# Performance work log

Measured on AMD Instinct MI355X. Metric: run time of the kernel, lower is better.

The kernel has to match this reference:

```python
import jax, jax.numpy as jnp
import numpy as np

N_NODES = 100000
N_GRAPHS = 256
N_EDGES = 800000


def gcn_conv(x, W, b, src, dst):
    """PyG GCNConv: self-loops + symmetric deg^-1/2 normalization + scatter-add."""
    h = x @ W  # [N, F_out]
    # degree on graph with self-loops (edge weight 1)
    deg = jax.ops.segment_sum(jnp.ones((src.shape[0],), h.dtype), dst,
                              num_segments=N_NODES) + 1.0
    dinv = jax.lax.rsqrt(deg)  # deg^-1/2, deg >= 1 so finite
    norm = dinv[src] * dinv[dst]  # [E]
    msg = h[src] * norm[:, None]  # gather + scale, [E, F_out]
    agg = jax.ops.segment_sum(msg, dst, num_segments=N_NODES)
    # self-loop contribution: dinv[i]^2 * h[i]
    agg = agg + h * (dinv * dinv)[:, None]
    return agg + b


def setup_inputs() -> dict:
    key = jax.random.key(0)
    ks = jax.random.split(key, 16)
    inp = {
        "x": jax.random.normal(ks[0], (N_NODES, 114), jnp.float32),
        "edge_index": jax.random.randint(ks[1], (2, N_EDGES), 0, N_NODES, jnp.int64)
        if jax.config.jax_enable_x64 else jax.random.randint(ks[1], (2, N_EDGES), 0, N_NODES, jnp.int32),
        "batch": jnp.sort(jax.random.randint(ks[2], (N_NODES,), 0, N_GRAPHS,
                                             jnp.int32)),
        "W1": jax.random.normal(ks[3], (114, 230), jnp.float32) * 0.09,
        "b1": jax.random.normal(ks[4], (230,), jnp.float32) * 0.01,
        "W2": jax.random.normal(ks[5], (230, 115), jnp.float32) * 0.07,
        "b2": jax.random.normal(ks[6], (115,), jnp.float32) * 0.01,
        "Wg": jax.random.normal(ks[7], (115, 64), jnp.float32) * 0.09,
        "bg": jax.random.normal(ks[8], (64,), jnp.float32) * 0.01,
        "Wf": jax.random.normal(ks[9], (64, 32), jnp.float32) * 0.12,
        "bf": jax.random.normal(ks[10], (32,), jnp.float32) * 0.01,
        "Wo": jax.random.normal(ks[11], (32, 1), jnp.float32) * 0.17,
        "bo": jax.random.normal(ks[12], (1,), jnp.float32) * 0.01,
    }
    return inp


def reference(x, edge_index, batch, W1, b1, W2, b2, Wg, bg, Wf, bf, Wo, bo):
    src, dst = edge_index[0], edge_index[1]
    h = jax.nn.relu(gcn_conv(x, W1, b1, src, dst))
    # dropout p=0.2 is identity at inference (training=False)
    h = jax.nn.relu(gcn_conv(h, W2, b2, src, dst))
    # global max pool over graphs; h >= 0 after relu so clamp empty segments to 0
    pooled = jax.ops.segment_max(h, batch, num_segments=N_GRAPHS)
    pooled = jnp.maximum(pooled, 0.0)  # [G, 115]
    g = jax.nn.relu(pooled @ Wg + bg)
    g = jax.nn.relu(g @ Wf + bf)
    return g @ Wo + bo  # [G, 1]
```

## Files before the change

kernel.cpp:

```cpp
#include <hip/hip_runtime.h>
#include <hip/hip_bf16.h>
#include <hip/hip_fp16.h>

#define NN 100000
#define NG 256
#define NE 800000

constexpr int F0 = 114;
constexpr int F1 = 230;
constexpr int F2 = 115;
constexpr int MPAD = 100096;

typedef _Float16 __attribute__((ext_vector_type(8))) f16x8;
typedef __attribute__((ext_vector_type(4))) float f32x4;
typedef __attribute__((ext_vector_type(8))) unsigned short u16x8;

__device__ __forceinline__ unsigned short f2h_bits(float x) {
  _Float16 h = (_Float16)x;
  return __builtin_bit_cast(unsigned short, h);
}
__device__ __forceinline__ float h_bits2f(unsigned short u) {
  return (float)__builtin_bit_cast(_Float16, u);
}


__global__ void k_count(const int* __restrict__ dst, int* __restrict__ cnt) {
  int e = blockIdx.x * blockDim.x + threadIdx.x;
  if (e < NE) atomicAdd(&cnt[dst[e]], 1);
}

__global__ void k_dinv(const int* __restrict__ cnt, float* __restrict__ dinv) {
  int i = blockIdx.x * blockDim.x + threadIdx.x;
  if (i < NN) dinv[i] = rsqrtf((float)cnt[i] + 1.0f);
}

constexpr int SCAN_T = 256;
constexpr int SCAN_E = 1024;
constexpr int NB = (NN + SCAN_E - 1) / SCAN_E;

__global__ void k_scan1(const int* __restrict__ cnt, int* __restrict__ off,
                        int* __restrict__ bsum) {
  __shared__ int s[SCAN_T];
  int b = blockIdx.x, t = threadIdx.x;
  int base = b * SCAN_E + t * 4;
  int v0 = 0, v1 = 0, v2 = 0, v3 = 0;
  if (base + 0 < NN) v0 = cnt[base + 0];
  if (base + 1 < NN) v1 = cnt[base + 1];
  if (base + 2 < NN) v2 = cnt[base + 2];
  if (base + 3 < NN) v3 = cnt[base + 3];
  int sum = v0 + v1 + v2 + v3;
  s[t] = sum;
  __syncthreads();
  for (int ofs = 1; ofs < SCAN_T; ofs <<= 1) {
    int x = (t >= ofs) ? s[t - ofs] : 0;
    __syncthreads();
    s[t] += x;
    __syncthreads();
  }
  int excl = s[t] - sum;
  if (base + 0 < NN) off[base + 0] = excl;
  if (base + 1 < NN) off[base + 1] = excl + v0;
  if (base + 2 < NN) off[base + 2] = excl + v0 + v1;
  if (base + 3 < NN) off[base + 3] = excl + v0 + v1 + v2;
  if (t == SCAN_T - 1) bsum[b] = s[t];
}

__global__ void k_scan2(int* bsum) {
  if (threadIdx.x == 0) {
    int run = 0;
    for (int i = 0; i < NB; ++i) { int v = bsum[i]; bsum[i] = run; run += v; }
  }
}

__global__ void k_scan3(int* __restrict__ off, const int* __restrict__ bsum,
                        int* __restrict__ cur) {
  int i = blockIdx.x * blockDim.x + threadIdx.x;
  if (i < NN) {
    int v = off[i] + bsum[i / SCAN_E];
    off[i] = v;
    cur[i] = v;
  }
  if (i == NN) off[NN] = NE;
}

__global__ void k_place(const int* __restrict__ src, const int* __restrict__ dst,
                        int* __restrict__ cur, int* __restrict__ srcs) {
  int e = blockIdx.x * blockDim.x + threadIdx.x;
  if (e >= NE) return;
  int p = atomicAdd(&cur[dst[e]], 1);
  srcs[p] = src[e];
}


__global__ void k_prepx(const float* __restrict__ x, const float* __restrict__ dinv,
                        unsigned short* __restrict__ xd) {
  int n = blockIdx.x, f = threadIdx.x;
  float v = (f < F0) ? x[(size_t)n * F0 + f] * dinv[n] : 0.0f;
  xd[(size_t)n * 128 + f] = f2h_bits(v);
}


template <bool POOL>
__global__ __launch_bounds__(256) void k_gatherw(
    const unsigned short* __restrict__ tab, const float* __restrict__ dinv,
    const int* __restrict__ off, const int* __restrict__ srcs,
    const float* __restrict__ b2, const int* __restrict__ batch,
    unsigned short* __restrict__ outh, float* __restrict__ pooled) {
  __shared__ float smax[4][128];
  __shared__ int sg[4];
  int w = threadIdx.x >> 6, lane = threadIdx.x & 63;
  int n = blockIdx.x * 4 + w;
  int grp = lane >> 4, sub = lane & 15;
  int fb = sub * 8;

  float acc[8] = {0.f, 0.f, 0.f, 0.f, 0.f, 0.f, 0.f, 0.f};
  int j0 = off[n], j1 = off[n + 1];
  for (int base = j0; base <= j1; base += 16) {
    int row[4];
    u16x8 v[4];
    bool has[4];
#pragma unroll
    for (int c = 0; c < 4; ++c) {
      int je = base + c * 4 + grp;
      row[c] = (je < j1) ? srcs[je] : ((je == j1) ? n : -1);
      has[c] = row[c] >= 0;
    }
#pragma unroll
    for (int c = 0; c < 4; ++c)
      if (has[c]) v[c] = *(const u16x8*)&tab[(size_t)row[c] * 128 + fb];
#pragma unroll
    for (int c = 0; c < 4; ++c)
      if (has[c]) {
#pragma unroll
        for (int u = 0; u < 8; ++u) acc[u] += h_bits2f(v[c][u]);
      }
  }
#pragma unroll
  for (int u = 0; u < 8; ++u) {
    acc[u] += __shfl_xor(acc[u], 16);
    acc[u] += __shfl_xor(acc[u], 32);
  }
  float dn = dinv[n];

  if constexpr (!POOL) {
    if (grp == 0) {
      u16x8 o;
#pragma unroll
      for (int u = 0; u < 8; ++u) o[u] = f2h_bits(acc[u] * dn);
      *(u16x8*)&outh[(size_t)n * 128 + fb] = o;
    }
  } else {
    if (grp == 0) {
#pragma unroll
      for (int u = 0; u < 8; ++u) {
        int f = fb + u;
        float bb = (f < F2) ? b2[f] : 0.0f;
        smax[w][f] = fmaxf(acc[u] * dn + bb, 0.0f);
      }
      if (sub == 0) sg[w] = batch[n];
    }
    __syncthreads();
    int t = threadIdx.x;
    if (t < 128) {
      int g0 = sg[0];
      bool same = (sg[1] == g0) & (sg[2] == g0) & (sg[3] == g0);
      if (same) {
        float m = fmaxf(fmaxf(smax[0][t], smax[1][t]),
                        fmaxf(smax[2][t], smax[3][t]));
        if (t < F2 && m > 0.0f)
          atomicMax((int*)&pooled[g0 * F2 + t], __float_as_int(m));
      } else {
        for (int ww = 0; ww < 4; ++ww) {
          float m = smax[ww][t];
          if (t < F2 && m > 0.0f)
            atomicMax((int*)&pooled[sg[ww] * F2 + t], __float_as_int(m));
        }
      }
    }
  }
}


__global__ void k_prepB(const float* __restrict__ W, unsigned short* __restrict__ Bh,
                        unsigned short* __restrict__ Bl, int K, int N, int KP) {
  int n = blockIdx.x, k = threadIdx.x;
  float v = (k < K && n < N) ? W[(size_t)k * N + n] : 0.0f;
  unsigned short h = f2h_bits(v);
  unsigned short l = f2h_bits(v - h_bits2f(h));
  Bh[(size_t)n * KP + k] = h;
  Bl[(size_t)n * KP + k] = l;
}


__global__ __launch_bounds__(256) void k_fused(
    const unsigned short* __restrict__ A,
    const unsigned short* __restrict__ B1h, const unsigned short* __restrict__ B1l,
    const unsigned short* __restrict__ B2h, const unsigned short* __restrict__ B2l,
    const float* __restrict__ b1, const float* __restrict__ dscale,
    unsigned short* __restrict__ td) {
  constexpr int LDH = 264;
  constexpr int LD = 72;
  __shared__ unsigned short h1s[64 * LDH];
  __shared__ unsigned short As[64 * LD];
  __shared__ unsigned short Bs[2][128 * LD];

  int t = threadIdx.x;
  int m0 = blockIdx.x * 64;
  int lane = t & 63, w = t >> 6;
  int r = lane & 15, kb = (lane >> 4) * 8;
  int rq = (lane >> 4) * 4;
  int wc = w * 32;

  int arow = t >> 2, aq = t & 3;
  int brow = t >> 1, bs = t & 1;

  for (int h = 0; h < 2; ++h) {
    f32x4 acc[4][2];
#pragma unroll
    for (int i = 0; i < 4; ++i)
#pragma unroll
      for (int j = 0; j < 2; ++j) acc[i][j] = (f32x4){0.f, 0.f, 0.f, 0.f};

    for (int kc = 0; kc < 2; ++kc) {
      __syncthreads();
      {
        size_t ga = (size_t)(m0 + arow) * 128 + kc * 64 + aq * 16;
        *(u16x8*)&As[arow * LD + aq * 16]     = *(const u16x8*)&A[ga];
        *(u16x8*)&As[arow * LD + aq * 16 + 8] = *(const u16x8*)&A[ga + 8];
        size_t gb = (size_t)(h * 128 + brow) * 128 + kc * 64 + bs * 32;
        int lo = brow * LD + bs * 32;
#pragma unroll
        for (int v = 0; v < 4; ++v) {
          *(u16x8*)&Bs[0][lo + v * 8] = *(const u16x8*)&B1h[gb + v * 8];
          *(u16x8*)&Bs[1][lo + v * 8] = *(const u16x8*)&B1l[gb + v * 8];
        }
      }
      __syncthreads();
#pragma unroll
      for (int ks = 0; ks < 2; ++ks) {
        int col = ks * 32 + kb;
        f16x8 a[4], bh[2], bl[2];
#pragma unroll
        for (int i = 0; i < 4; ++i) a[i] = *(const f16x8*)&As[(i * 16 + r) * LD + col];
#pragma unroll
        for (int j = 0; j < 2; ++j) {
          bh[j] = *(const f16x8*)&Bs[0][(wc + j * 16 + r) * LD + col];
          bl[j] = *(const f16x8*)&Bs[1][(wc + j * 16 + r) * LD + col];
        }
#pragma unroll
        for (int i = 0; i < 4; ++i)
#pragma unroll
          for (int j = 0; j < 2; ++j)
            acc[i][j] = __builtin_amdgcn_mfma_f32_16x16x32_f16(a[i], bl[j], acc[i][j], 0, 0, 0);
#pragma unroll
        for (int i = 0; i < 4; ++i)
#pragma unroll
          for (int j = 0; j < 2; ++j)
            acc[i][j] = __builtin_amdgcn_mfma_f32_16x16x32_f16(a[i], bh[j], acc[i][j], 0, 0, 0);
      }
    }
#pragma unroll
    for (int i = 0; i < 4; ++i)
#pragma unroll
      for (int j = 0; j < 2; ++j) {
        int nl = wc + j * 16 + r;
        int n = h * 128 + nl;
        float bb = (n < F1) ? b1[n] : 0.0f;
#pragma unroll
        for (int q = 0; q < 4; ++q) {
          int ml = i * 16 + rq + q;
          float v = (n < F1) ? fmaxf(acc[i][j][q] + bb, 0.0f) : 0.0f;
          h1s[ml * LDH + n] = f2h_bits(v);
        }
      }
  }

  f32x4 acc2[4][2];
#pragma unroll
  for (int i = 0; i < 4; ++i)
#pragma unroll
    for (int j = 0; j < 2; ++j) acc2[i][j] = (f32x4){0.f, 0.f, 0.f, 0.f};

  for (int kc = 0; kc < 4; ++kc) {
    __syncthreads();
    {
      size_t gb = (size_t)brow * 256 + kc * 64 + bs * 32;
      int lo = brow * LD + bs * 32;
#pragma unroll
      for (int v = 0; v < 4; ++v) {
        *(u16x8*)&Bs[0][lo + v * 8] = *(const u16x8*)&B2h[gb + v * 8];
        *(u16x8*)&Bs[1][lo + v * 8] = *(const u16x8*)&B2l[gb + v * 8];
      }
    }
    __syncthreads();
#pragma unroll
    for (int ks = 0; ks < 2; ++ks) {
      int colA = kc * 64 + ks * 32 + kb;
      int colB = ks * 32 + kb;
      f16x8 a[4], bh[2], bl[2];
#pragma unroll
      for (int i = 0; i < 4; ++i) a[i] = *(const f16x8*)&h1s[(i * 16 + r) * LDH + colA];
#pragma unroll
      for (int j = 0; j < 2; ++j) {
        bh[j] = *(const f16x8*)&Bs[0][(wc + j * 16 + r) * LD + colB];
        bl[j] = *(const f16x8*)&Bs[1][(wc + j * 16 + r) * LD + colB];
      }
#pragma unroll
      for (int i = 0; i < 4; ++i)
#pragma unroll
        for (int j = 0; j < 2; ++j)
          acc2[i][j] = __builtin_amdgcn_mfma_f32_16x16x32_f16(a[i], bl[j], acc2[i][j], 0, 0, 0);
#pragma unroll
      for (int i = 0; i < 4; ++i)
#pragma unroll
        for (int j = 0; j < 2; ++j)
          acc2[i][j] = __builtin_amdgcn_mfma_f32_16x16x32_f16(a[i], bh[j], acc2[i][j], 0, 0, 0);
    }
  }

  __syncthreads();
  constexpr int SW = 136;
  unsigned short* sw = h1s;
#pragma unroll
  for (int i = 0; i < 4; ++i)
#pragma unroll
    for (int j = 0; j < 2; ++j) {
      int nl = wc + j * 16 + r;
#pragma unroll
      for (int q = 0; q < 4; ++q) {
        int ml = i * 16 + rq + q;
        float v = acc2[i][j][q] * dscale[m0 + ml];
        sw[ml * SW + nl] = f2h_bits(v);
      }
    }
  __syncthreads();
  {
    int row = t >> 2, sgm = t & 3;
    const unsigned short* s = &sw[row * SW + sgm * 32];
    size_t dst = (size_t)(m0 + row) * 128 + sgm * 32;
#pragma unroll
    for (int v = 0; v < 4; ++v)
      *(u16x8*)&td[dst + v * 8] = *(const u16x8*)&s[v * 8];
  }
}


__global__ void k_mlp(const float* __restrict__ pooled,
                      const float* __restrict__ Wg, const float* __restrict__ bg,
                      const float* __restrict__ Wf, const float* __restrict__ bf,
                      const float* __restrict__ Wo, const float* __restrict__ bo,
                      float* __restrict__ out) {
  __shared__ float sp[F2];
  __shared__ float sg[64];
  __shared__ float sf[32];
  int g = blockIdx.x, t = threadIdx.x;
  for (int f = t; f < F2; f += 64) sp[f] = pooled[g * F2 + f];
  __syncthreads();
  float a = bg[t];
  for (int k = 0; k < F2; ++k) a += sp[k] * Wg[k * 64 + t];
  sg[t] = fmaxf(a, 0.0f);
  __syncthreads();
  if (t < 32) {
    float c = bf[t];
    for (int k = 0; k < 64; ++k) c += sg[k] * Wf[k * 32 + t];
    sf[t] = fmaxf(c, 0.0f);
  }
  __syncthreads();
  if (t == 0) {
    float c = bo[0];
    for (int k = 0; k < 32; ++k) c += sf[k] * Wo[k];
    out[g] = c;
  }
}


extern "C" void kernel_launch(void* const* d_in, const int* in_sizes, int n_in,
                              void* d_out, int out_size, void* d_ws, size_t ws_size,
                              hipStream_t stream) {
  const float* x  = (const float*)d_in[0];
  const int* ei   = (const int*)d_in[1];
  const int* batch = (const int*)d_in[2];
  const float* W1 = (const float*)d_in[3];
  const float* b1 = (const float*)d_in[4];
  const float* W2 = (const float*)d_in[5];
  const float* b2 = (const float*)d_in[6];
  const float* Wg = (const float*)d_in[7];
  const float* bg = (const float*)d_in[8];
  const float* Wf = (const float*)d_in[9];
  const float* bf = (const float*)d_in[10];
  const float* Wo = (const float*)d_in[11];
  const float* bo = (const float*)d_in[12];
  const int* src = ei;
  const int* dst = ei + NE;

  char* p = (char*)d_ws;
  auto alloc4 = [&](size_t units) { void* r = p; p += units * 4; return r; };
  float* dinv  = (float*)alloc4(100224);
  int* cnt     = (int*)alloc4(100224);
  int* off     = (int*)alloc4(100352);
  int* cur     = (int*)alloc4(100224);
  int* bsum    = (int*)alloc4(128);
  int* srcs    = (int*)alloc4(NE);
  unsigned short* xd   = (unsigned short*)alloc4((size_t)NN * 128 / 2);
  unsigned short* aggX = (unsigned short*)alloc4((size_t)MPAD * 128 / 2);
  unsigned short* td   = (unsigned short*)alloc4((size_t)MPAD * 128 / 2);
  unsigned short* Bt1h = (unsigned short*)alloc4(256 * 128 / 2);
  unsigned short* Bt1l = (unsigned short*)alloc4(256 * 128 / 2);
  unsigned short* Bt2h = (unsigned short*)alloc4(128 * 256 / 2);
  unsigned short* Bt2l = (unsigned short*)alloc4(128 * 256 / 2);
  float* pooled = (float*)alloc4((size_t)NG * F2);

  hipMemsetAsync(cnt, 0, 100224 * sizeof(int), stream);
  hipMemsetAsync(pooled, 0, (size_t)NG * F2 * sizeof(float), stream);

  k_count<<<(NE + 255) / 256, 256, 0, stream>>>(dst, cnt);
  k_dinv<<<(NN + 255) / 256, 256, 0, stream>>>(cnt, dinv);
  k_scan1<<<NB, SCAN_T, 0, stream>>>(cnt, off, bsum);
  k_scan2<<<1, 64, 0, stream>>>(bsum);
  k_scan3<<<(NN + 256) / 256, 256, 0, stream>>>(off, bsum, cur);
  k_place<<<(NE + 255) / 256, 256, 0, stream>>>(src, dst, cur, srcs);

  k_prepB<<<256, 128, 0, stream>>>(W1, Bt1h, Bt1l, F0, F1, 128);
  k_prepB<<<128, 256, 0, stream>>>(W2, Bt2h, Bt2l, F1, F2, 256);

  k_prepx<<<NN, 128, 0, stream>>>(x, dinv, xd);
  k_gatherw<false><<<NN / 4, 256, 0, stream>>>(xd, dinv, off, srcs,
                                               nullptr, nullptr, aggX, nullptr);

  k_fused<<<MPAD / 64, 256, 0, stream>>>(aggX, Bt1h, Bt1l, Bt2h, Bt2l,
                                         b1, dinv, td);

  k_gatherw<true><<<NN / 4, 256, 0, stream>>>(td, dinv, off, srcs,
                                              b2, batch, nullptr, pooled);

  k_mlp<<<NG, 64, 0, stream>>>(pooled, Wg, bg, Wf, bf, Wo, bo, (float*)d_out);
}
```

Measured before the change: 307.9 us.

## Restructure fused GEMM with register-prefetched B tiles, swizzled LDS, and interleaved layer-2 chunks

The fused two-layer GEMM kernel is rewritten. B tiles are prefetched into registers one stage ahead, and A fragments are loaded directly from global memory into registers instead of being staged through LDS. Each 128-column half of layer 1 now feeds straight into the matching slice of the layer-2 reduction, so the h1 buffer only holds 128 columns. LDS use drops to 48KB with an XOR swizzle replacing padding, and launch bounds now request 3 blocks per CU for occupancy; the serial single-thread block-sum scan also becomes a wave-shuffle scan. The risks are higher register pressure from the prefetch buffers and more barriers.

```diff
diff --git a/kernel.cpp b/kernel.cpp
--- a/kernel.cpp
+++ b/kernel.cpp
@@ -66,10 +66,18 @@
 }
 
 __global__ void k_scan2(int* bsum) {
-  if (threadIdx.x == 0) {
-    int run = 0;
-    for (int i = 0; i < NB; ++i) { int v = bsum[i]; bsum[i] = run; run += v; }
-  }
+  __shared__ int ws[2];
+  int t = threadIdx.x;
+  int v = (t < NB) ? bsum[t] : 0;
+  int orig = v;
+  for (int o = 1; o < 64; o <<= 1) {
+    int x = __shfl_up(v, o, 64);
+    if ((t & 63) >= o) v += x;
+  }
+  if ((t & 63) == 63) ws[t >> 6] = v;
+  __syncthreads();
+  if (t >= 64) v += ws[0];
+  if (t < NB) bsum[t] = v - orig;
 }
 
 __global__ void k_scan3(int* __restrict__ off, const int* __restrict__ bsum,
@@ -192,155 +200,189 @@
 }
 
 
-__global__ __launch_bounds__(256) void k_fused(
+__global__ __launch_bounds__(256, 3) void k_fused(
     const unsigned short* __restrict__ A,
     const unsigned short* __restrict__ B1h, const unsigned short* __restrict__ B1l,
     const unsigned short* __restrict__ B2h, const unsigned short* __restrict__ B2l,
     const float* __restrict__ b1, const float* __restrict__ dscale,
     unsigned short* __restrict__ td) {
-  constexpr int LDH = 264;
-  constexpr int LD = 72;
-  __shared__ unsigned short h1s[64 * LDH];
-  __shared__ unsigned short As[64 * LD];
-  __shared__ unsigned short Bs[2][128 * LD];
-
-  int t = threadIdx.x;
-  int m0 = blockIdx.x * 64;
-  int lane = t & 63, w = t >> 6;
-  int r = lane & 15, kb = (lane >> 4) * 8;
-  int rq = (lane >> 4) * 4;
-  int wc = w * 32;
-
-  int arow = t >> 2, aq = t & 3;
-  int brow = t >> 1, bs = t & 1;
-
-  for (int h = 0; h < 2; ++h) {
-    f32x4 acc[4][2];
+  __shared__ char lds[49152];
+  char* h1B = lds;
+  char* Bs0 = lds + 16384;
+  char* Bs1 = lds + 32768;
+
+  const int t = threadIdx.x;
+  const int m0 = blockIdx.x * 64;
+  const int lane = t & 63, w = t >> 6;
+  const int r = lane & 15;
+  const int kq = lane >> 4;
+  const int kb2 = kq * 16;
+  const int kbu = kq * 8;
+  const int rq = kq * 4;
+  const int wc = w * 32;
+  const int brow = t >> 1, bseg = t & 1;
+  const int rb = brow * 128, swb = (brow & 7) << 4;
+
+  const unsigned short* Ath = A + (size_t)(m0 + r) * 128 + kbu;
+
+  u16x8 Ph[4], Pl[4];
+  f16x8 a[4][2];
+  f32x4 acc[4][2], acc2[4][2];
+#pragma unroll
+  for (int i = 0; i < 4; ++i)
+#pragma unroll
+    for (int j = 0; j < 2; ++j) {
+      acc[i][j] = (f32x4){0.f, 0.f, 0.f, 0.f};
+      acc2[i][j] = (f32x4){0.f, 0.f, 0.f, 0.f};
+    }
+
+  auto issueB = [&](const unsigned short* Gh, const unsigned short* Gl, size_t base) {
+#pragma unroll
+    for (int v = 0; v < 4; ++v) {
+      Ph[v] = *(const u16x8*)&Gh[base + v * 8];
+      Pl[v] = *(const u16x8*)&Gl[base + v * 8];
+    }
+  };
+  auto commitB = [&]() {
+#pragma unroll
+    for (int v = 0; v < 4; ++v) {
+      const int bo = (bseg * 64 + v * 16) ^ swb;
+      *(u16x8*)(Bs0 + rb + bo) = Ph[v];
+      *(u16x8*)(Bs1 + rb + bo) = Pl[v];
+    }
+  };
+  auto loadA = [&](int kc) {
 #pragma unroll
     for (int i = 0; i < 4; ++i)
 #pragma unroll
+      for (int ks = 0; ks < 2; ++ks)
+        a[i][ks] = *(const f16x8*)&Ath[i * 2048 + kc * 64 + ks * 32];
+  };
+  auto mfma1 = [&]() {
+#pragma unroll
+    for (int ks = 0; ks < 2; ++ks) {
+      f16x8 bh[2], bl[2];
+#pragma unroll
+      for (int j = 0; j < 2; ++j) {
+        const int row = wc + j * 16 + r;
+        const int bo = (ks * 64 + kb2) ^ ((row & 7) << 4);
+        bh[j] = *(const f16x8*)(Bs0 + row * 128 + bo);
+        bl[j] = *(const f16x8*)(Bs1 + row * 128 + bo);
+      }
+#pragma unroll
+      for (int i = 0; i < 4; ++i)
+#pragma unroll
+        for (int j = 0; j < 2; ++j)
+          acc[i][j] = __builtin_amdgcn_mfma_f32_16x16x32_f16(a[i][ks], bl[j], acc[i][j], 0, 0, 0);
+#pragma unroll
+      for (int i = 0; i < 4; ++i)
+#pragma unroll
+        for (int j = 0; j < 2; ++j)
+          acc[i][j] = __builtin_amdgcn_mfma_f32_16x16x32_f16(a[i][ks], bh[j], acc[i][j], 0, 0, 0);
+    }
+  };
+  auto mfma2 = [&](int kc) {
+#pragma unroll
+    for (int ks = 0; ks < 2; ++ks) {
+      f16x8 ah[4], bh[2], bl[2];
+#pragma unroll
+      for (int i = 0; i < 4; ++i) {
+        const int row = i * 16 + r;
+        ah[i] = *(const f16x8*)(h1B + row * 256 +
+                                ((kc * 128 + ks * 64 + kb2) ^ ((row & 7) << 4)));
+      }
+#pragma unroll
+      for (int j = 0; j < 2; ++j) {
+        const int row = wc + j * 16 + r;
+        const int bo = (ks * 64 + kb2) ^ ((row & 7) << 4);
+        bh[j] = *(const f16x8*)(Bs0 + row * 128 + bo);
+        bl[j] = *(const f16x8*)(Bs1 + row * 128 + bo);
+      }
+#pragma unroll
+      for (int i = 0; i < 4; ++i)
+#pragma unroll
+        for (int j = 0; j < 2; ++j)
+          acc2[i][j] = __builtin_amdgcn_mfma_f32_16x16x32_f16(ah[i], bl[j], acc2[i][j], 0, 0, 0);
+#pragma unroll
+      for (int i = 0; i < 4; ++i)
+#pragma unroll
+        for (int j = 0; j < 2; ++j)
+          acc2[i][j] = __builtin_amdgcn_mfma_f32_16x16x32_f16(ah[i], bh[j], acc2[i][j], 0, 0, 0);
+    }
+  };
+  auto writeH1 = [&](int h) {
+#pragma unroll
+    for (int i = 0; i < 4; ++i)
+#pragma unroll
+      for (int j = 0; j < 2; ++j) {
+        const int nl = wc + j * 16 + r;
+        const int n = h * 128 + nl;
+        const bool val = n < F1;
+        const float bb = val ? b1[n] : 0.0f;
+#pragma unroll
+        for (int q = 0; q < 4; ++q) {
+          const int ml = i * 16 + rq + q;
+          const float v = val ? fmaxf(acc[i][j][q] + bb, 0.0f) : 0.0f;
+          *(unsigned short*)(h1B + ml * 256 + ((nl * 2) ^ ((ml & 7) << 4))) = f2h_bits(v);
+        }
+      }
+  };
+  auto zacc = [&]() {
+#pragma unroll
+    for (int i = 0; i < 4; ++i)
+#pragma unroll
       for (int j = 0; j < 2; ++j) acc[i][j] = (f32x4){0.f, 0.f, 0.f, 0.f};
-
-    for (int kc = 0; kc < 2; ++kc) {
-      __syncthreads();
-      {
-        size_t ga = (size_t)(m0 + arow) * 128 + kc * 64 + aq * 16;
-        *(u16x8*)&As[arow * LD + aq * 16]     = *(const u16x8*)&A[ga];
-        *(u16x8*)&As[arow * LD + aq * 16 + 8] = *(const u16x8*)&A[ga + 8];
-        size_t gb = (size_t)(h * 128 + brow) * 128 + kc * 64 + bs * 32;
-        int lo = brow * LD + bs * 32;
-#pragma unroll
-        for (int v = 0; v < 4; ++v) {
-          *(u16x8*)&Bs[0][lo + v * 8] = *(const u16x8*)&B1h[gb + v * 8];
-          *(u16x8*)&Bs[1][lo + v * 8] = *(const u16x8*)&B1l[gb + v * 8];
-        }
-      }
-      __syncthreads();
-#pragma unroll
-      for (int ks = 0; ks < 2; ++ks) {
-        int col = ks * 32 + kb;
-        f16x8 a[4], bh[2], bl[2];
-#pragma unroll
-        for (int i = 0; i < 4; ++i) a[i] = *(const f16x8*)&As[(i * 16 + r) * LD + col];
-#pragma unroll
-        for (int j = 0; j < 2; ++j) {
-          bh[j] = *(const f16x8*)&Bs[0][(wc + j * 16 + r) * LD + col];
-          bl[j] = *(const f16x8*)&Bs[1][(wc + j * 16 + r) * LD + col];
-        }
-#pragma unroll
-        for (int i = 0; i < 4; ++i)
-#pragma unroll
-          for (int j = 0; j < 2; ++j)
-            acc[i][j] = __builtin_amdgcn_mfma_f32_16x16x32_f16(a[i], bl[j], acc[i][j], 0, 0, 0);
-#pragma unroll
-        for (int i = 0; i < 4; ++i)
-#pragma unroll
-          for (int j = 0; j < 2; ++j)
-            acc[i][j] = __builtin_amdgcn_mfma_f32_16x16x32_f16(a[i], bh[j], acc[i][j], 0, 0, 0);
-      }
-    }
-#pragma unroll
-    for (int i = 0; i < 4; ++i)
-#pragma unroll
-      for (int j = 0; j < 2; ++j) {
-        int nl = wc + j * 16 + r;
-        int n = h * 128 + nl;
-        float bb = (n < F1) ? b1[n] : 0.0f;
-#pragma unroll
-        for (int q = 0; q < 4; ++q) {
-          int ml = i * 16 + rq + q;
-          float v = (n < F1) ? fmaxf(acc[i][j][q] + bb, 0.0f) : 0.0f;
-          h1s[ml * LDH + n] = f2h_bits(v);
-        }
-      }
-  }
-
-  f32x4 acc2[4][2];
+  };
+  auto B1BASE = [&](int h, int kc) {
+    return (size_t)(h * 128 + brow) * 128 + kc * 64 + bseg * 32;
+  };
+  auto B2BASE = [&](int h, int kc) {
+    return (size_t)brow * 256 + h * 128 + kc * 64 + bseg * 32;
+  };
+
+  issueB(B1h, B1l, B1BASE(0, 0));
+
+  commitB(); loadA(0); issueB(B1h, B1l, B1BASE(0, 1));
+  __syncthreads(); mfma1();
+  __syncthreads(); commitB(); loadA(1); issueB(B2h, B2l, B2BASE(0, 0));
+  __syncthreads(); mfma1(); writeH1(0);
+  __syncthreads(); commitB(); issueB(B2h, B2l, B2BASE(0, 1));
+  __syncthreads(); mfma2(0);
+  __syncthreads(); commitB(); issueB(B1h, B1l, B1BASE(1, 0));
+  __syncthreads(); mfma2(1);
+  zacc();
+  __syncthreads(); commitB(); loadA(0); issueB(B1h, B1l, B1BASE(1, 1));
+  __syncthreads(); mfma1();
+  __syncthreads(); commitB(); loadA(1); issueB(B2h, B2l, B2BASE(1, 0));
+  __syncthreads(); mfma1(); writeH1(1);
+  __syncthreads(); commitB(); issueB(B2h, B2l, B2BASE(1, 1));
+  __syncthreads(); mfma2(0);
+  __syncthreads(); commitB();
+  __syncthreads(); mfma2(1);
+
+  __syncthreads();
 #pragma unroll
   for (int i = 0; i < 4; ++i)
 #pragma unroll
-    for (int j = 0; j < 2; ++j) acc2[i][j] = (f32x4){0.f, 0.f, 0.f, 0.f};
-
-  for (int kc = 0; kc < 4; ++kc) {
-    __syncthreads();
-    {
-      size_t gb = (size_t)brow * 256 + kc * 64 + bs * 32;
-      int lo = brow * LD + bs * 32;
-#pragma unroll
-      for (int v = 0; v < 4; ++v) {
-        *(u16x8*)&Bs[0][lo + v * 8] = *(const u16x8*)&B2h[gb + v * 8];
-        *(u16x8*)&Bs[1][lo + v * 8] = *(const u16x8*)&B2l[gb + v * 8];
-      }
-    }
-    __syncthreads();
-#pragma unroll
-    for (int ks = 0; ks < 2; ++ks) {
-      int colA = kc * 64 + ks * 32 + kb;
-      int colB = ks * 32 + kb;
-      f16x8 a[4], bh[2], bl[2];
-#pragma unroll
-      for (int i = 0; i < 4; ++i) a[i] = *(const f16x8*)&h1s[(i * 16 + r) * LDH + colA];
-#pragma unroll
-      for (int j = 0; j < 2; ++j) {
-        bh[j] = *(const f16x8*)&Bs[0][(wc + j * 16 + r) * LD + colB];
-        bl[j] = *(const f16x8*)&Bs[1][(wc + j * 16 + r) * LD + colB];
-      }
-#pragma unroll
-      for (int i = 0; i < 4; ++i)
-#pragma unroll
-        for (int j = 0; j < 2; ++j)
-          acc2[i][j] = __builtin_amdgcn_mfma_f32_16x16x32_f16(a[i], bl[j], acc2[i][j], 0, 0, 0);
-#pragma unroll
-      for (int i = 0; i < 4; ++i)
-#pragma unroll
-        for (int j = 0; j < 2; ++j)
-          acc2[i][j] = __builtin_amdgcn_mfma_f32_16x16x32_f16(a[i], bh[j], acc2[i][j], 0, 0, 0);
-    }
-  }
-
-  __syncthreads();
-  constexpr int SW = 136;
-  unsigned short* sw = h1s;
-#pragma unroll
-  for (int i = 0; i < 4; ++i)
-#pragma unroll
     for (int j = 0; j < 2; ++j) {
-      int nl = wc + j * 16 + r;
+      const int nl = wc + j * 16 + r;
 #pragma unroll
       for (int q = 0; q < 4; ++q) {
-        int ml = i * 16 + rq + q;
-        float v = acc2[i][j][q] * dscale[m0 + ml];
-        sw[ml * SW + nl] = f2h_bits(v);
+        const int ml = i * 16 + rq + q;
+        const float v = acc2[i][j][q] * dscale[m0 + ml];
+        *(unsigned short*)(h1B + ml * 256 + ((nl * 2) ^ ((ml & 7) << 4))) = f2h_bits(v);
       }
     }
   __syncthreads();
   {
-    int row = t >> 2, sgm = t & 3;
-    const unsigned short* s = &sw[row * SW + sgm * 32];
-    size_t dst = (size_t)(m0 + row) * 128 + sgm * 32;
-#pragma unroll
-    for (int v = 0; v < 4; ++v)
-      *(u16x8*)&td[dst + v * 8] = *(const u16x8*)&s[v * 8];
+    const int row = t >> 2, seg = t & 3;
+    const int swz = (row & 7) << 4;
+    const size_t dst = (size_t)(m0 + row) * 128 + seg * 32;
+#pragma unroll
+    for (int v = 0; v < 4; ++v) {
+      u16x8 d = *(const u16x8*)(h1B + row * 256 + ((seg * 64 + v * 16) ^ swz));
+      *(u16x8*)&td[dst + v * 8] = d;
+    }
   }
 }
 
@@ -416,7 +458,7 @@
   k_count<<<(NE + 255) / 256, 256, 0, stream>>>(dst, cnt);
   k_dinv<<<(NN + 255) / 256, 256, 0, stream>>>(cnt, dinv);
   k_scan1<<<NB, SCAN_T, 0, stream>>>(cnt, off, bsum);
-  k_scan2<<<1, 64, 0, stream>>>(bsum);
+  k_scan2<<<1, 128, 0, stream>>>(bsum);
   k_scan3<<<(NN + 256) / 256, 256, 0, stream>>>(off, bsum, cur);
   k_place<<<(NE + 255) / 256, 256, 0, stream>>>(src, dst, cur, srcs);
 
```

Measured after the change: 352.3 us. 1.14x slower.
